# Performance work log

Measured on AMD Instinct MI355X. Metric: run time of the kernel, lower is better.

## Reference

```python
import jax, jax.numpy as jnp
import numpy as np

B, S, D_MODEL, D_K = 4, 4096, 1024, 64


def setup_inputs() -> dict:
    key = jax.random.key(0)
    ks = jax.random.split(key, 4)
    scale = 1.0 / np.sqrt(D_MODEL)
    x = jax.random.normal(ks[0], (B, S, D_MODEL), dtype=jnp.float32)
    Wq = jax.random.normal(ks[1], (D_MODEL, D_K), dtype=jnp.float32) * scale
    Wk = jax.random.normal(ks[2], (D_MODEL, D_K), dtype=jnp.float32) * scale
    Wv = jax.random.normal(ks[3], (D_MODEL, D_K), dtype=jnp.float32) * scale
    bq = jnp.zeros((D_K,), dtype=jnp.float32)
    bk = jnp.zeros((D_K,), dtype=jnp.float32)
    bv = jnp.zeros((D_K,), dtype=jnp.float32)
    # causal mask: 1 = keep, 0 = masked (matches docstring semantics)
    mask = jnp.broadcast_to(
        jnp.tril(jnp.ones((S, S), dtype=jnp.int32))[None], (B, S, S)
    )
    return {"x": x, "mask": mask, "Wq": Wq, "bq": bq, "Wk": Wk, "bk": bk, "Wv": Wv, "bv": bv}


def reference(x, mask, Wq, bq, Wk, bk, Wv, bv):
    # Q/K/V projections: (B, S, d_model) @ (d_model, d_k) -> (B, S, d_k)
    Q = jnp.einsum("bsd,dk->bsk", x, Wq) + bq
    K = jnp.einsum("bsd,dk->bsk", x, Wk) + bk
    V = jnp.einsum("bsd,dk->bsk", x, Wv) + bv
    # scaled dot-product scores: (B, S, S)
    scores = jnp.einsum("bqk,bsk->bqs", Q, K) / jnp.sqrt(jnp.float32(D_K))
    scores = jnp.where(mask == 0, jnp.float32(-jnp.inf), scores)
    attn = jax.nn.softmax(scores, axis=-1)
    # dropout with p_drop = 0.0 is identity
    out = jnp.einsum("bqs,bsk->bqk", attn, V)  # (B, S, d_k)
    return out
```

## Files before the change

### kernel.cpp

```cpp
#include <hip/hip_runtime.h>
#include <hip/hip_bf16.h>


typedef float  f32x4 __attribute__((ext_vector_type(4)));
typedef short  s16x8 __attribute__((ext_vector_type(8)));
typedef short  s16x4 __attribute__((ext_vector_type(4)));

#define MFMA16(A, B, C) __builtin_amdgcn_mfma_f32_16x16x32_bf16((A), (B), (C), 0, 0, 0)

static __device__ __forceinline__ ushort f2bf(float f) {
    union { float f; unsigned u; } v; v.f = f;
    unsigned u = v.u;
    unsigned r = (u + 0x7FFFu + ((u >> 16) & 1u)) >> 16;
    return (ushort)r;
}

static __device__ __forceinline__ f32x4 fzero() {
    f32x4 v; v[0] = v[1] = v[2] = v[3] = 0.f; return v;
}

__global__ __launch_bounds__(256) void prep_w(const float* __restrict__ Wq,
                                              const float* __restrict__ Wk,
                                              const float* __restrict__ Wv,
                                              short* __restrict__ Wt) {
    const int c = blockIdx.x;
    const int t = threadIdx.x;
    const float* src; int cc; float sc = 1.0f;
    if (c < 64)       { src = Wq; cc = c;       sc = 0.125f; }
    else if (c < 128) { src = Wk; cc = c - 64;  }
    else              { src = Wv; cc = c - 128; }
    const int k0 = t * 4;
    s16x4 o;
    #pragma unroll
    for (int i = 0; i < 4; ++i) o[i] = (short)f2bf(src[(size_t)(k0 + i) * 64 + cc] * sc);
    *(s16x4*)&Wt[(size_t)c * 1024 + k0] = o;
}

__global__ __launch_bounds__(256) void proj(const float* __restrict__ x,
                                            const short* __restrict__ Wt,
                                            const float* __restrict__ bq,
                                            const float* __restrict__ bk,
                                            const float* __restrict__ bv,
                                            short* __restrict__ Qb,
                                            short* __restrict__ Kb,
                                            short* __restrict__ Vt) {
    const int tid  = threadIdx.x;
    const int lane = tid & 63;
    const int w    = tid >> 6;
    const int m0   = blockIdx.x * 32;
    const int l15  = lane & 15, gr = lane >> 4;

    __shared__ short xs[2][32][136];

    const int srow = tid >> 3;
    const int sc8  = tid & 7;
    const float* sbase = x + (size_t)(m0 + srow) * 1024 + 4 * sc8;

    f32x4 acc[3][2];
    #pragma unroll
    for (int m = 0; m < 3; ++m)
        for (int n = 0; n < 2; ++n) acc[m][n] = fzero();

    const short* aptr = Wt + (size_t)(48 * w + l15) * 1024 + 8 * gr;

    f32x4 ld[4];
    #pragma unroll
    for (int i = 0; i < 4; ++i) ld[i] = *(const f32x4*)(sbase + 32 * i);
    #pragma unroll
    for (int i = 0; i < 4; ++i) {
        s16x4 o;
        #pragma unroll
        for (int j = 0; j < 4; ++j) o[j] = (short)f2bf(ld[i][j]);
        *(s16x4*)&xs[0][srow][4 * sc8 + 32 * i] = o;
    }
    __syncthreads();

    for (int c = 0; c < 8; ++c) {
        const int buf = c & 1;
        if (c < 7) {
            #pragma unroll
            for (int i = 0; i < 4; ++i) ld[i] = *(const f32x4*)(sbase + 128 * (c + 1) + 32 * i);
        }
        #pragma unroll
        for (int f = 0; f < 4; ++f) {
            const int ko = 128 * c + 32 * f;
            s16x8 a[3];
            #pragma unroll
            for (int m = 0; m < 3; ++m) a[m] = *(const s16x8*)(aptr + (size_t)m * 16 * 1024 + ko);
            s16x8 b[2];
            #pragma unroll
            for (int n = 0; n < 2; ++n) b[n] = *(const s16x8*)&xs[buf][16 * n + l15][32 * f + 8 * gr];
            #pragma unroll
            for (int m = 0; m < 3; ++m)
                for (int n = 0; n < 2; ++n) acc[m][n] = MFMA16(a[m], b[n], acc[m][n]);
        }
        if (c < 7) {
            #pragma unroll
            for (int i = 0; i < 4; ++i) {
                s16x4 o;
                #pragma unroll
                for (int j = 0; j < 4; ++j) o[j] = (short)f2bf(ld[i][j]);
                *(s16x4*)&xs[buf ^ 1][srow][4 * sc8 + 32 * i] = o;
            }
        }
        __syncthreads();
    }

    #pragma unroll
    for (int m = 0; m < 3; ++m) {
        const int c0 = 48 * w + 16 * m + 4 * gr;
        #pragma unroll
        for (int n = 0; n < 2; ++n) {
            const int row = m0 + 16 * n + l15;
            f32x4 v = acc[m][n];
            if (c0 < 64) {
                s16x4 o;
                #pragma unroll
                for (int r = 0; r < 4; ++r) o[r] = (short)f2bf(v[r] + 0.125f * bq[c0 + r]);
                *(s16x4*)&Qb[(size_t)row * 64 + c0] = o;
            } else if (c0 < 128) {
                s16x4 o;
                #pragma unroll
                for (int r = 0; r < 4; ++r) o[r] = (short)f2bf(v[r] + bk[c0 - 64 + r]);
                *(s16x4*)&Kb[(size_t)row * 64 + (c0 - 64)] = o;
            } else {
                const int b = row >> 12, s = row & 4095;
                #pragma unroll
                for (int r = 0; r < 4; ++r)
                    Vt[((size_t)b * 64 + (c0 - 128 + r)) * 4096 + s] =
                        (short)f2bf(v[r] + bv[c0 - 128 + r]);
            }
        }
    }
}

__global__ __launch_bounds__(256) void attn(const short* __restrict__ Qb,
                                            const short* __restrict__ Kb,
                                            const short* __restrict__ Vt,
                                            float* __restrict__ out) {
    const int bid   = blockIdx.x;
    const int batch = bid & 3;
    const int g     = 127 - (bid >> 2);
    const int q0    = g * 32;
    const int tid   = threadIdx.x, lane = tid & 63, w = tid >> 6;
    const int l15   = lane & 15, gr = lane >> 4;

    __shared__ short P_lds[4][32][72];
    __shared__ float Om[4][32][64];
    __shared__ float Mm[4][32], Lm[4][32];

    const size_t qrow0 = (size_t)batch * 4096;

    s16x8 qf[2][2];
    #pragma unroll
    for (int ms = 0; ms < 2; ++ms)
        for (int f = 0; f < 2; ++f)
            qf[ms][f] = *(const s16x8*)&Qb[(qrow0 + q0 + 16 * ms + l15) * 64 + 32 * f + 8 * gr];

    f32x4 o[2][4];
    float mreg[2][4], lreg[2][4];
    #pragma unroll
    for (int ms = 0; ms < 2; ++ms) {
        for (int n = 0; n < 4; ++n) o[ms][n] = fzero();
        for (int r = 0; r < 4; ++r) { mreg[ms][r] = -1e30f; lreg[ms][r] = 0.f; }
    }

    const int L  = q0 + 32;
    const int nt = (L + 63) >> 6;
    const int t0 = (nt * w) >> 2, t1 = (nt * (w + 1)) >> 2;

    const short* Kbase = Kb + qrow0 * 64;
    const short* Vbase = Vt + (size_t)batch * 64 * 4096;

    for (int t = t0; t < t1; ++t) {
        const int j0 = t << 6;
        s16x8 kf[4][2], vf[4][2];
        #pragma unroll
        for (int n = 0; n < 4; ++n)
            for (int f = 0; f < 2; ++f) {
                kf[n][f] = *(const s16x8*)&Kbase[(size_t)(j0 + 16 * n + l15) * 64 + 32 * f + 8 * gr];
                vf[n][f] = *(const s16x8*)&Vbase[(size_t)(16 * n + l15) * 4096 + j0 + 32 * f + 8 * gr];
            }

        const bool needmask = (j0 + 63 > q0);
        #pragma unroll
        for (int ms = 0; ms < 2; ++ms) {
            f32x4 s[4];
            #pragma unroll
            for (int n = 0; n < 4; ++n) {
                s[n] = fzero();
                for (int f = 0; f < 2; ++f) s[n] = MFMA16(qf[ms][f], kf[n][f], s[n]);
            }
            if (needmask) {
                const int qrow = q0 + 16 * ms + 4 * gr;
                #pragma unroll
                for (int n = 0; n < 4; ++n) {
                    const int j = j0 + 16 * n + l15;
                    for (int r = 0; r < 4; ++r)
                        if (j > qrow + r) s[n][r] = -1e30f;
                }
            }
            float tm[4];
            #pragma unroll
            for (int r = 0; r < 4; ++r)
                tm[r] = fmaxf(fmaxf(s[0][r], s[1][r]), fmaxf(s[2][r], s[3][r]));
            #pragma unroll
            for (int d = 1; d < 16; d <<= 1)
                for (int r = 0; r < 4; ++r) tm[r] = fmaxf(tm[r], __shfl_xor(tm[r], d));

            float p[4][4];
            #pragma unroll
            for (int r = 0; r < 4; ++r) {
                const float mn = fmaxf(mreg[ms][r], tm[r]);
                const float sc = __expf(mreg[ms][r] - mn);
                mreg[ms][r] = mn;
                lreg[ms][r] *= sc;
                for (int n = 0; n < 4; ++n) o[ms][n][r] *= sc;
                float ls = 0.f;
                for (int n = 0; n < 4; ++n) { float e = __expf(s[n][r] - mn); p[n][r] = e; ls += e; }
                lreg[ms][r] += ls;
            }
            #pragma unroll
            for (int n = 0; n < 4; ++n)
                for (int r = 0; r < 4; ++r)
                    P_lds[w][16 * ms + 4 * gr + r][16 * n + l15] = (short)f2bf(p[n][r]);
        }
        #pragma unroll
        for (int ms = 0; ms < 2; ++ms) {
            s16x8 pf[2];
            for (int f = 0; f < 2; ++f)
                pf[f] = *(const s16x8*)&P_lds[w][16 * ms + l15][32 * f + 8 * gr];
            #pragma unroll
            for (int n = 0; n < 4; ++n)
                for (int f = 0; f < 2; ++f)
                    o[ms][n] = MFMA16(pf[f], vf[n][f], o[ms][n]);
        }
    }

    #pragma unroll
    for (int ms = 0; ms < 2; ++ms)
        for (int d = 1; d < 16; d <<= 1)
            for (int r = 0; r < 4; ++r) lreg[ms][r] += __shfl_xor(lreg[ms][r], d);

    #pragma unroll
    for (int ms = 0; ms < 2; ++ms) {
        for (int n = 0; n < 4; ++n)
            for (int r = 0; r < 4; ++r)
                Om[w][16 * ms + 4 * gr + r][16 * n + l15] = o[ms][n][r];
        if (l15 == 0)
            for (int r = 0; r < 4; ++r) {
                Mm[w][16 * ms + 4 * gr + r] = mreg[ms][r];
                Lm[w][16 * ms + 4 * gr + r] = lreg[ms][r];
            }
    }
    __syncthreads();

    {
        const int r  = tid >> 3;
        const int d0 = (tid & 7) * 8;
        const float mt = fmaxf(fmaxf(Mm[0][r], Mm[1][r]), fmaxf(Mm[2][r], Mm[3][r]));
        float lt = 0.f;
        f32x4 a0 = fzero(), a1 = fzero();
        #pragma unroll
        for (int ww = 0; ww < 4; ++ww) {
            const float sc = __expf(Mm[ww][r] - mt);
            lt += sc * Lm[ww][r];
            f32x4 v0 = *(const f32x4*)&Om[ww][r][d0];
            f32x4 v1 = *(const f32x4*)&Om[ww][r][d0 + 4];
            #pragma unroll
            for (int j = 0; j < 4; ++j) { a0[j] += sc * v0[j]; a1[j] += sc * v1[j]; }
        }
        const float inv = 1.f / lt;
        const size_t ob = (qrow0 + q0 + r) * 64 + d0;
        f32x4 r0, r1;
        #pragma unroll
        for (int j = 0; j < 4; ++j) { r0[j] = a0[j] * inv; r1[j] = a1[j] * inv; }
        *(f32x4*)&out[ob]     = r0;
        *(f32x4*)&out[ob + 4] = r1;
    }
}

extern "C" void kernel_launch(void* const* d_in, const int* in_sizes, int n_in,
                              void* d_out, int out_size, void* d_ws, size_t ws_size,
                              hipStream_t stream) {
    const float* x  = (const float*)d_in[0];
    const float* Wq = (const float*)d_in[2];
    const float* bq = (const float*)d_in[3];
    const float* Wk = (const float*)d_in[4];
    const float* bk = (const float*)d_in[5];
    const float* Wv = (const float*)d_in[6];
    const float* bv = (const float*)d_in[7];
    float* out = (float*)d_out;

    char* ws = (char*)d_ws;
    short* Wt = (short*)(ws);
    short* Qb = (short*)(ws + 393216);
    short* Kb = (short*)(ws + 2490368);
    short* Vt = (short*)(ws + 4587520);

    prep_w<<<dim3(192), dim3(256), 0, stream>>>(Wq, Wk, Wv, Wt);
    proj<<<dim3(512), dim3(256), 0, stream>>>(x, Wt, bq, bk, bv, Qb, Kb, Vt);
    attn<<<dim3(512), dim3(256), 0, stream>>>(Qb, Kb, Vt, out);
}
```

Before: 91.18 us.

## Rewrite attention inner loop with 32x32 MFMA, transposed scores, register-only P

Switches the attention kernel from 16x16x32 to 32x32x16 bf16 MFMA and computes the transposed score tile S^T = K·Q^T. Each lane then holds a full query column, so the row max and sum need only one cross-half shuffle. P is packed to bf16 with v_cvt_pk_bf16_f32 and rearranged with v_permlane32_swap instead of a round trip through LDS, and KV tiles shrink to 32 so masking applies only on the diagonal tile. It also swizzles the block-to-batch mapping, pads the Om LDS buffer and sets launch_bounds occupancy to 2. The cost is more complex register layouts and reliance on gfx950-specific inline assembly.

```diff
diff --git a/kernel.cpp b/kernel.cpp
--- a/kernel.cpp
+++ b/kernel.cpp
@@ -2,11 +2,13 @@
 #include <hip/hip_bf16.h>
 
 
-typedef float  f32x4 __attribute__((ext_vector_type(4)));
-typedef short  s16x8 __attribute__((ext_vector_type(8)));
-typedef short  s16x4 __attribute__((ext_vector_type(4)));
+typedef float  f32x4  __attribute__((ext_vector_type(4)));
+typedef float  f32x16 __attribute__((ext_vector_type(16)));
+typedef short  s16x8  __attribute__((ext_vector_type(8)));
+typedef short  s16x4  __attribute__((ext_vector_type(4)));
 
 #define MFMA16(A, B, C) __builtin_amdgcn_mfma_f32_16x16x32_bf16((A), (B), (C), 0, 0, 0)
+#define MFMA32(A, B, C) __builtin_amdgcn_mfma_f32_32x32x16_bf16((A), (B), (C), 0, 0, 0)
 
 static __device__ __forceinline__ ushort f2bf(float f) {
     union { float f; unsigned u; } v; v.f = f;
@@ -134,144 +136,128 @@
     }
 }
 
-__global__ __launch_bounds__(256) void attn(const short* __restrict__ Qb,
-                                            const short* __restrict__ Kb,
-                                            const short* __restrict__ Vt,
-                                            float* __restrict__ out) {
+__global__ __launch_bounds__(256, 2) void attn(const short* __restrict__ Qb,
+                                               const short* __restrict__ Kb,
+                                               const short* __restrict__ Vt,
+                                               float* __restrict__ out) {
     const int bid   = blockIdx.x;
-    const int batch = bid & 3;
-    const int g     = 127 - (bid >> 2);
+    const int wgid  = (bid & 7) * 64 + (bid >> 3);
+    const int batch = wgid >> 7;
+    const int g     = 127 - (wgid & 127);
     const int q0    = g * 32;
     const int tid   = threadIdx.x, lane = tid & 63, w = tid >> 6;
-    const int l15   = lane & 15, gr = lane >> 4;
-
-    __shared__ short P_lds[4][32][72];
-    __shared__ float Om[4][32][64];
+    const int l31   = lane & 31, h = lane >> 5, kb = 4 * h;
+
+    __shared__ float Om[4][32][68];
     __shared__ float Mm[4][32], Lm[4][32];
 
-    const size_t qrow0 = (size_t)batch * 4096;
-
-    s16x8 qf[2][2];
-    #pragma unroll
-    for (int ms = 0; ms < 2; ++ms)
-        for (int f = 0; f < 2; ++f)
-            qf[ms][f] = *(const s16x8*)&Qb[(qrow0 + q0 + 16 * ms + l15) * 64 + 32 * f + 8 * gr];
-
-    f32x4 o[2][4];
-    float mreg[2][4], lreg[2][4];
-    #pragma unroll
-    for (int ms = 0; ms < 2; ++ms) {
-        for (int n = 0; n < 4; ++n) o[ms][n] = fzero();
-        for (int r = 0; r < 4; ++r) { mreg[ms][r] = -1e30f; lreg[ms][r] = 0.f; }
-    }
-
-    const int L  = q0 + 32;
-    const int nt = (L + 63) >> 6;
+    const size_t row0 = (size_t)batch * 4096;
+
+    const short* Qp = Qb + (row0 + q0 + l31) * 64 + 8 * h;
+    s16x8 qf[4];
+    #pragma unroll
+    for (int kk = 0; kk < 4; ++kk) qf[kk] = *(const s16x8*)(Qp + 16 * kk);
+
+    f32x16 oT0, oT1;
+    #pragma unroll
+    for (int r = 0; r < 16; ++r) { oT0[r] = 0.f; oT1[r] = 0.f; }
+    float m = -1e30f, l_ = 0.f;
+
+    const int nt = g + 1;
     const int t0 = (nt * w) >> 2, t1 = (nt * (w + 1)) >> 2;
 
-    const short* Kbase = Kb + qrow0 * 64;
-    const short* Vbase = Vt + (size_t)batch * 64 * 4096;
+    const short* Kp = Kb + (row0 + l31) * 64 + 8 * h;
+    const short* Vp = Vt + ((size_t)batch * 64 + l31) * 4096 + 8 * h;
 
     for (int t = t0; t < t1; ++t) {
-        const int j0 = t << 6;
-        s16x8 kf[4][2], vf[4][2];
-        #pragma unroll
-        for (int n = 0; n < 4; ++n)
-            for (int f = 0; f < 2; ++f) {
-                kf[n][f] = *(const s16x8*)&Kbase[(size_t)(j0 + 16 * n + l15) * 64 + 32 * f + 8 * gr];
-                vf[n][f] = *(const s16x8*)&Vbase[(size_t)(16 * n + l15) * 4096 + j0 + 32 * f + 8 * gr];
+        const int j0 = t * 32;
+        s16x8 kf[4], va[2][2];
+        #pragma unroll
+        for (int kk = 0; kk < 4; ++kk)
+            kf[kk] = *(const s16x8*)(Kp + (size_t)j0 * 64 + 16 * kk);
+        #pragma unroll
+        for (int dt = 0; dt < 2; ++dt)
+            #pragma unroll
+            for (int kk = 0; kk < 2; ++kk)
+                va[dt][kk] = *(const s16x8*)(Vp + (size_t)dt * 32 * 4096 + j0 + 16 * kk);
+
+        f32x16 sacc;
+        #pragma unroll
+        for (int r = 0; r < 16; ++r) sacc[r] = 0.f;
+        #pragma unroll
+        for (int kk = 0; kk < 4; ++kk) sacc = MFMA32(kf[kk], qf[kk], sacc);
+
+        if (j0 == q0) {
+            #pragma unroll
+            for (int r = 0; r < 16; ++r) {
+                const int kvloc = (r & 3) + 8 * (r >> 2) + kb;
+                if (kvloc > l31) sacc[r] = -1e30f;
             }
-
-        const bool needmask = (j0 + 63 > q0);
-        #pragma unroll
-        for (int ms = 0; ms < 2; ++ms) {
-            f32x4 s[4];
-            #pragma unroll
-            for (int n = 0; n < 4; ++n) {
-                s[n] = fzero();
-                for (int f = 0; f < 2; ++f) s[n] = MFMA16(qf[ms][f], kf[n][f], s[n]);
-            }
-            if (needmask) {
-                const int qrow = q0 + 16 * ms + 4 * gr;
-                #pragma unroll
-                for (int n = 0; n < 4; ++n) {
-                    const int j = j0 + 16 * n + l15;
-                    for (int r = 0; r < 4; ++r)
-                        if (j > qrow + r) s[n][r] = -1e30f;
-                }
-            }
-            float tm[4];
-            #pragma unroll
-            for (int r = 0; r < 4; ++r)
-                tm[r] = fmaxf(fmaxf(s[0][r], s[1][r]), fmaxf(s[2][r], s[3][r]));
-            #pragma unroll
-            for (int d = 1; d < 16; d <<= 1)
-                for (int r = 0; r < 4; ++r) tm[r] = fmaxf(tm[r], __shfl_xor(tm[r], d));
-
-            float p[4][4];
-            #pragma unroll
-            for (int r = 0; r < 4; ++r) {
-                const float mn = fmaxf(mreg[ms][r], tm[r]);
-                const float sc = __expf(mreg[ms][r] - mn);
-                mreg[ms][r] = mn;
-                lreg[ms][r] *= sc;
-                for (int n = 0; n < 4; ++n) o[ms][n][r] *= sc;
-                float ls = 0.f;
-                for (int n = 0; n < 4; ++n) { float e = __expf(s[n][r] - mn); p[n][r] = e; ls += e; }
-                lreg[ms][r] += ls;
-            }
-            #pragma unroll
-            for (int n = 0; n < 4; ++n)
-                for (int r = 0; r < 4; ++r)
-                    P_lds[w][16 * ms + 4 * gr + r][16 * n + l15] = (short)f2bf(p[n][r]);
-        }
-        #pragma unroll
-        for (int ms = 0; ms < 2; ++ms) {
-            s16x8 pf[2];
-            for (int f = 0; f < 2; ++f)
-                pf[f] = *(const s16x8*)&P_lds[w][16 * ms + l15][32 * f + 8 * gr];
-            #pragma unroll
-            for (int n = 0; n < 4; ++n)
-                for (int f = 0; f < 2; ++f)
-                    o[ms][n] = MFMA16(pf[f], vf[n][f], o[ms][n]);
-        }
-    }
-
-    #pragma unroll
-    for (int ms = 0; ms < 2; ++ms)
-        for (int d = 1; d < 16; d <<= 1)
-            for (int r = 0; r < 4; ++r) lreg[ms][r] += __shfl_xor(lreg[ms][r], d);
-
-    #pragma unroll
-    for (int ms = 0; ms < 2; ++ms) {
-        for (int n = 0; n < 4; ++n)
-            for (int r = 0; r < 4; ++r)
-                Om[w][16 * ms + 4 * gr + r][16 * n + l15] = o[ms][n][r];
-        if (l15 == 0)
-            for (int r = 0; r < 4; ++r) {
-                Mm[w][16 * ms + 4 * gr + r] = mreg[ms][r];
-                Lm[w][16 * ms + 4 * gr + r] = lreg[ms][r];
-            }
-    }
+        }
+
+        float sm = sacc[0];
+        #pragma unroll
+        for (int r = 1; r < 16; ++r) sm = fmaxf(sm, sacc[r]);
+        sm = fmaxf(sm, __shfl_xor(sm, 32));
+        const float mn = fmaxf(m, sm);
+        const float sc = __expf(m - mn);
+        m = mn;
+
+        float p[16]; float ls = 0.f;
+        #pragma unroll
+        for (int r = 0; r < 16; ++r) { p[r] = __expf(sacc[r] - mn); ls += p[r]; }
+        l_ = l_ * sc + ls + __shfl_xor(ls, 32);
+        #pragma unroll
+        for (int r = 0; r < 16; ++r) { oT0[r] *= sc; oT1[r] *= sc; }
+
+        unsigned pw[8];
+        #pragma unroll
+        for (int i = 0; i < 8; ++i)
+            asm("v_cvt_pk_bf16_f32 %0, %1, %2" : "=v"(pw[i]) : "v"(p[2 * i]), "v"(p[2 * i + 1]));
+        asm volatile("v_permlane32_swap_b32 %0, %1" : "+v"(pw[0]), "+v"(pw[2]));
+        asm volatile("v_permlane32_swap_b32 %0, %1" : "+v"(pw[1]), "+v"(pw[3]));
+        asm volatile("v_permlane32_swap_b32 %0, %1" : "+v"(pw[4]), "+v"(pw[6]));
+        asm volatile("v_permlane32_swap_b32 %0, %1" : "+v"(pw[5]), "+v"(pw[7]));
+        union { unsigned u[4]; s16x8 v; } f0, f1;
+        f0.u[0] = pw[0]; f0.u[1] = pw[1]; f0.u[2] = pw[2]; f0.u[3] = pw[3];
+        f1.u[0] = pw[4]; f1.u[1] = pw[5]; f1.u[2] = pw[6]; f1.u[3] = pw[7];
+
+        oT0 = MFMA32(va[0][0], f0.v, oT0);
+        oT0 = MFMA32(va[0][1], f1.v, oT0);
+        oT1 = MFMA32(va[1][0], f0.v, oT1);
+        oT1 = MFMA32(va[1][1], f1.v, oT1);
+    }
+
+    #pragma unroll
+    for (int rg = 0; rg < 4; ++rg) {
+        f32x4 v0, v1;
+        #pragma unroll
+        for (int j = 0; j < 4; ++j) { v0[j] = oT0[4 * rg + j]; v1[j] = oT1[4 * rg + j]; }
+        const int d0 = rg * 8 + kb;
+        *(f32x4*)&Om[w][l31][d0]      = v0;
+        *(f32x4*)&Om[w][l31][32 + d0] = v1;
+    }
+    if (lane < 32) { Mm[w][l31] = m; Lm[w][l31] = l_; }
     __syncthreads();
 
     {
-        const int r  = tid >> 3;
-        const int d0 = (tid & 7) * 8;
-        const float mt = fmaxf(fmaxf(Mm[0][r], Mm[1][r]), fmaxf(Mm[2][r], Mm[3][r]));
-        float lt = 0.f;
+        const int q = tid >> 3, d0 = (tid & 7) * 8;
+        const float m0 = Mm[0][q], m1 = Mm[1][q], m2 = Mm[2][q], m3 = Mm[3][q];
+        const float mt = fmaxf(fmaxf(m0, m1), fmaxf(m2, m3));
+        float sw[4];
+        sw[0] = __expf(m0 - mt); sw[1] = __expf(m1 - mt);
+        sw[2] = __expf(m2 - mt); sw[3] = __expf(m3 - mt);
+        const float lt = sw[0] * Lm[0][q] + sw[1] * Lm[1][q] + sw[2] * Lm[2][q] + sw[3] * Lm[3][q];
+        const float inv = 1.f / lt;
         f32x4 a0 = fzero(), a1 = fzero();
         #pragma unroll
         for (int ww = 0; ww < 4; ++ww) {
-            const float sc = __expf(Mm[ww][r] - mt);
-            lt += sc * Lm[ww][r];
-            f32x4 v0 = *(const f32x4*)&Om[ww][r][d0];
-            f32x4 v1 = *(const f32x4*)&Om[ww][r][d0 + 4];
-            #pragma unroll
-            for (int j = 0; j < 4; ++j) { a0[j] += sc * v0[j]; a1[j] += sc * v1[j]; }
-        }
-        const float inv = 1.f / lt;
-        const size_t ob = (qrow0 + q0 + r) * 64 + d0;
+            f32x4 u0 = *(const f32x4*)&Om[ww][q][d0];
+            f32x4 u1 = *(const f32x4*)&Om[ww][q][d0 + 4];
+            #pragma unroll
+            for (int j = 0; j < 4; ++j) { a0[j] += sw[ww] * u0[j]; a1[j] += sw[ww] * u1[j]; }
+        }
+        const size_t ob = (row0 + q0 + q) * 64 + d0;
         f32x4 r0, r1;
         #pragma unroll
         for (int j = 0; j < 4; ++j) { r0[j] = a0[j] * inv; r1[j] = a1[j] * inv; }
```

Result: slower. 94.09 us (+3.2%).
